# Performance work log

Measured on AMD Instinct MI355X. Metric: run time of the kernel, lower is better.

The kernel has to match this reference:

```python
import jax, jax.numpy as jnp
import numpy as np

B, S, H, D = 8, 1024, 16, 64
W = H * D  # hidden width = 1024


def setup_inputs() -> dict:
    key = jax.random.key(0)
    ks = jax.random.split(key, 5)
    std = 0.02
    return {
        "from_tensor": jax.random.normal(ks[0], (B, S, W), dtype=jnp.float32),
        "to_tensor": jax.random.normal(ks[1], (B, S, W), dtype=jnp.float32),
        "Wq": jax.random.normal(ks[2], (W, W), dtype=jnp.float32) * std,
        "bq": jnp.zeros((W,), dtype=jnp.float32),
        "Wk": jax.random.normal(ks[3], (W, W), dtype=jnp.float32) * std,
        "bk": jnp.zeros((W,), dtype=jnp.float32),
        "Wv": jax.random.normal(ks[4], (W, W), dtype=jnp.float32) * std,
        "bv": jnp.zeros((W,), dtype=jnp.float32),
    }


def reference(from_tensor, to_tensor, Wq, bq, Wk, bk, Wv, bv):
    # Q/K/V projections (no activations: query_act=key_act=value_act=None)
    q = from_tensor @ Wq + bq  # [B, S, W]
    k = to_tensor @ Wk + bk
    v = to_tensor @ Wv + bv
    # split heads -> [B, H, S, D]
    q = q.reshape(B, S, H, D).transpose(0, 2, 1, 3)
    k = k.reshape(B, S, H, D).transpose(0, 2, 1, 3)
    v = v.reshape(B, S, H, D).transpose(0, 2, 1, 3)
    scale = 1.0 / np.sqrt(float(D))
    scores = jnp.einsum("bhqd,bhkd->bhqk", q, k) * scale  # [B, H, S, S]
    # attention_mask=None, dropout_prob=0.0 -> no mask, no dropout
    probs = jax.nn.softmax(scores, axis=-1)
    ctx = jnp.einsum("bhqk,bhkd->bhqd", probs, v)  # [B, H, S, D]
    # merge heads -> [B, S, H*D] (do_return_2d_tensor=False)
    return ctx.transpose(0, 2, 1, 3).reshape(B, S, H * D)
```

## Files before the change

kernel.cpp:

```cpp
#include <hip/hip_runtime.h>
#include <hip/hip_bf16.h>
#include <math.h>


#define B_ 8
#define S_ 1024
#define H_ 16
#define D_ 64
#define W_ 1024

typedef __bf16 bf16x8 __attribute__((ext_vector_type(8)));
typedef float f32x4 __attribute__((ext_vector_type(4)));
typedef unsigned short ushort_t;

#define MFMA16(a, b, c) __builtin_amdgcn_mfma_f32_16x16x32_bf16((a), (b), (c), 0, 0, 0)

__device__ inline ushort_t f2bf(float f) {
    unsigned int u = __float_as_uint(f);
    u += 0x7fff + ((u >> 16) & 1);
    return (ushort_t)(u >> 16);
}

__device__ inline unsigned f2bf_rhu_u(float f) {
    return (__float_as_uint(f) + 0x8000u) >> 16;
}

__device__ inline void async16(const void* g, void* l) {
    __builtin_amdgcn_global_load_lds((const __attribute__((address_space(1))) void*)g,
                                     (__attribute__((address_space(3))) void*)l, 16, 0, 0);
}

__global__ __launch_bounds__(256) void prep(const float* __restrict__ from,
                                            const float* __restrict__ to_,
                                            const float* __restrict__ Wq,
                                            const float* __restrict__ Wk,
                                            const float* __restrict__ Wv,
                                            ushort_t* __restrict__ fromB,
                                            ushort_t* __restrict__ toB,
                                            ushort_t* __restrict__ Wt, int n4) {
    int z = blockIdx.y;
    int t = threadIdx.x;
    if (z < 2) {
        int i = blockIdx.x * 256 + t;
        if (i >= n4) return;
        const float* src = z ? to_ : from;
        ushort_t* dst = z ? toB : fromB;
        float4 v = ((const float4*)src)[i];
        ushort4 o;
        o.x = f2bf(v.x); o.y = f2bf(v.y); o.z = f2bf(v.z); o.w = f2bf(v.w);
        ((ushort4*)dst)[i] = o;
        return;
    }
    int bx = blockIdx.x;
    if (bx >= 3072) return;
    __shared__ float tile[32][33];
    int zz = bx >> 10;
    int tl = bx & 1023;
    int bxx = tl & 31, byy = tl >> 5;
    const float* src = (zz == 0) ? Wq : (zz == 1 ? Wk : Wv);
    ushort_t* dst = Wt + (size_t)zz * W_ * W_;
    int tx = t & 31, ty = t >> 5;
    int x = bxx * 32 + tx;
#pragma unroll
    for (int jj = 0; jj < 4; jj++) {
        int y = byy * 32 + ty + jj * 8;
        tile[ty + jj * 8][tx] = src[(size_t)y * W_ + x];
    }
    __syncthreads();
    int x2 = byy * 32 + tx;
#pragma unroll
    for (int jj = 0; jj < 4; jj++) {
        int y2 = bxx * 32 + ty + jj * 8;
        dst[(size_t)y2 * W_ + x2] = f2bf(tile[tx][ty + jj * 8]);
    }
}

__global__ __launch_bounds__(256) void qkv_gemm(const ushort_t* __restrict__ fromB,
                                                const ushort_t* __restrict__ toB,
                                                const ushort_t* __restrict__ Wt,
                                                const float* __restrict__ bq,
                                                const float* __restrict__ bk,
                                                const float* __restrict__ bv,
                                                ushort_t* __restrict__ Qd,
                                                ushort_t* __restrict__ Kd,
                                                ushort_t* __restrict__ Vt) {
    __shared__ __attribute__((aligned(16))) ushort_t As[128 * 32];
    __shared__ __attribute__((aligned(16))) ushort_t Bs[128 * 32];
    int z = blockIdx.y;
    const ushort_t* A = (z == 0) ? fromB : toB;
    const ushort_t* Bt = Wt + (size_t)z * (W_ * W_);
    const float* bias = (z == 0) ? bq : (z == 1 ? bk : bv);
    ushort_t* dst = (z == 0) ? Qd : (z == 1 ? Kd : Vt);

    int bx = blockIdx.x;
    int j64 = bx >> 3;
    int mTile = ((bx & 7) << 3) | (j64 >> 3);
    int nTile = j64 & 7;
    int mBase = mTile * 128, nBase = nTile * 128;

    int t = threadIdx.x;
    int lane = t & 63, w = t >> 6;
    int wm = w >> 1, wn = w & 1;
    int ln = lane & 15, qd = lane >> 4;
    int wb = t & ~63;

    f32x4 zero = {0.f, 0.f, 0.f, 0.f};
    f32x4 acc[4][4];
#pragma unroll
    for (int i = 0; i < 4; i++)
#pragma unroll
        for (int j = 0; j < 4; j++) acc[i][j] = zero;

    for (int kt = 0; kt < 32; ++kt) {
        int k0 = kt * 32;
#pragma unroll
        for (int c = 0; c < 2; ++c) {
            int idx16 = c * 256 + t;
            int row = idx16 >> 2, seg = idx16 & 3;
            async16(A + (size_t)(mBase + row) * W_ + k0 + seg * 8, As + (size_t)(c * 256 + wb) * 8);
            async16(Bt + (size_t)(nBase + row) * W_ + k0 + seg * 8, Bs + (size_t)(c * 256 + wb) * 8);
        }
        __syncthreads();
        bf16x8 af[4], bfr[4];
#pragma unroll
        for (int i = 0; i < 4; i++) af[i] = *(const bf16x8*)(As + (wm * 64 + i * 16 + ln) * 32 + qd * 8);
#pragma unroll
        for (int j = 0; j < 4; j++) bfr[j] = *(const bf16x8*)(Bs + (wn * 64 + j * 16 + ln) * 32 + qd * 8);
#pragma unroll
        for (int i = 0; i < 4; i++)
#pragma unroll
            for (int j = 0; j < 4; j++) acc[i][j] = MFMA16(af[i], bfr[j], acc[i][j]);
        __syncthreads();
    }

#pragma unroll
    for (int j = 0; j < 4; j++) {
        int n = nBase + wn * 64 + j * 16 + ln;
        float bb = bias[n];
        int h = n >> 6, d = n & 63;
#pragma unroll
        for (int i = 0; i < 4; i++) {
            int mrow = mBase + wm * 64 + i * 16 + qd * 4;
#pragma unroll
            for (int r = 0; r < 4; r++) {
                int m = mrow + r;
                int b = m >> 10, s = m & 1023;
                float v = acc[i][j][r] + bb;
                if (z == 0) v *= 0.18033688011111773f;
                size_t idx;
                if (z < 2) idx = ((size_t)(b * H_ + h) * S_ + s) * D_ + d;
                else {
                    int sp = (s & ~63) | (s & 0x23) | ((s & 0x0C) << 1) | ((s & 0x10) >> 2);
                    idx = ((size_t)(b * H_ + h) * D_ + d) * S_ + sp;
                }
                dst[idx] = f2bf(v);
            }
        }
    }
}

__global__ __launch_bounds__(256, 4) void attn(const ushort_t* __restrict__ Qd,
                                               const ushort_t* __restrict__ Kd,
                                               const ushort_t* __restrict__ Vt,
                                               float* __restrict__ out) {
    __shared__ __attribute__((aligned(16))) ushort_t Ks[2][4096];
    __shared__ __attribute__((aligned(16))) ushort_t Vs[2][4096];

    int L = blockIdx.x;
    int bh = ((L & 7) << 4) | ((L >> 3) & 15);
    int qx = L >> 7;
    int t = threadIdx.x, w = t >> 6, lane = t & 63;
    int ln = lane & 15, qd = lane >> 4;
    int qbase = qx * 128 + w * 32;
    const ushort_t* Qb = Qd + (size_t)bh * S_ * D_;
    const ushort_t* Kb = Kd + (size_t)bh * S_ * D_;
    const ushort_t* Vb = Vt + (size_t)bh * D_ * S_;

    bf16x8 qf[2][2];
#pragma unroll
    for (int i = 0; i < 2; i++) {
        const ushort_t* qp = Qb + (size_t)(qbase + i * 16 + ln) * D_ + qd * 8;
        qf[i][0] = *(const bf16x8*)qp;
        qf[i][1] = *(const bf16x8*)(qp + 32);
    }

    int l8 = lane >> 3, s8 = lane & 7;
    int stgOff = (s8 ^ l8) << 3;
    const ushort_t* kg = Kb + (size_t)(w * 16 + l8) * D_ + stgOff;
    const ushort_t* vg = Vb + (size_t)(w * 16 + l8) * S_ + stgOff;
    int kOff = ln * 64 + ((qd ^ (ln & 7)) << 3);

    float rs[2] = {0.f, 0.f};
    f32x4 zero = {0.f, 0.f, 0.f, 0.f};
    f32x4 accO[2][4];
#pragma unroll
    for (int i = 0; i < 2; i++)
#pragma unroll
        for (int jd = 0; jd < 4; jd++) accO[i][jd] = zero;

    async16(kg, &Ks[0][w * 1024]);
    async16(kg + 8 * D_, &Ks[0][w * 1024 + 512]);
    async16(vg, &Vs[0][w * 1024]);
    async16(vg + 8 * S_, &Vs[0][w * 1024 + 512]);

    for (int c = 0; c < 16; ++c) {
        int buf = c & 1;
        __builtin_amdgcn_s_waitcnt(0x0F70);
        __syncthreads();
        if (c + 1 < 16) {
            int kc = (c + 1) * 64;
            async16(kg + (size_t)kc * D_, &Ks[buf ^ 1][w * 1024]);
            async16(kg + (size_t)kc * D_ + 8 * D_, &Ks[buf ^ 1][w * 1024 + 512]);
            async16(vg + kc, &Vs[buf ^ 1][w * 1024]);
            async16(vg + kc + 8 * S_, &Vs[buf ^ 1][w * 1024 + 512]);
        }

        f32x4 sc[2][4];
#pragma unroll
        for (int i = 0; i < 2; i++)
#pragma unroll
            for (int j = 0; j < 4; j++) sc[i][j] = zero;
        __builtin_amdgcn_s_setprio(1);
#pragma unroll
        for (int j = 0; j < 4; j++) {
            bf16x8 k0 = *(const bf16x8*)&Ks[buf][j * 1024 + kOff];
            bf16x8 k1 = *(const bf16x8*)&Ks[buf][(j * 1024 + kOff) ^ 32];
#pragma unroll
            for (int i = 0; i < 2; i++) {
                sc[i][j] = MFMA16(k0, qf[i][0], sc[i][j]);
                sc[i][j] = MFMA16(k1, qf[i][1], sc[i][j]);
            }
        }
        __builtin_amdgcn_s_setprio(0);

        bf16x8 pfrag[2][2];
#pragma unroll
        for (int i = 0; i < 2; i++)
#pragma unroll
            for (int m = 0; m < 2; m++) {
                union { unsigned u[4]; bf16x8 v; } pk;
#pragma unroll
                for (int jh = 0; jh < 2; jh++) {
                    float p0 = exp2f(sc[i][2 * m + jh][0]);
                    float p1 = exp2f(sc[i][2 * m + jh][1]);
                    float p2 = exp2f(sc[i][2 * m + jh][2]);
                    float p3 = exp2f(sc[i][2 * m + jh][3]);
                    rs[i] += (p0 + p1) + (p2 + p3);
                    pk.u[jh * 2]     = f2bf_rhu_u(p0) | (f2bf_rhu_u(p1) << 16);
                    pk.u[jh * 2 + 1] = f2bf_rhu_u(p2) | (f2bf_rhu_u(p3) << 16);
                }
                pfrag[i][m] = pk.v;
            }

        __builtin_amdgcn_s_setprio(1);
#pragma unroll
        for (int dt = 0; dt < 4; dt++)
#pragma unroll
            for (int m = 0; m < 2; m++) {
                bf16x8 vf = *(const bf16x8*)&Vs[buf][(dt * 16 + ln) * 64 +
                                                    ((((m << 2) + qd) ^ (ln & 7)) << 3)];
                accO[0][dt] = MFMA16(vf, pfrag[0][m], accO[0][dt]);
                accO[1][dt] = MFMA16(vf, pfrag[1][m], accO[1][dt]);
            }
        __builtin_amdgcn_s_setprio(0);
    }

    float inv[2];
#pragma unroll
    for (int i = 0; i < 2; i++) {
        float s = rs[i];
        s += __shfl_xor(s, 16);
        s += __shfl_xor(s, 32);
        inv[i] = 1.f / s;
    }
    int b = bh >> 4, h = bh & 15;
#pragma unroll
    for (int i = 0; i < 2; i++) {
        int q = qbase + i * 16 + ln;
        float* op = out + ((size_t)(b * S_ + q) * H_ + h) * D_ + qd * 4;
#pragma unroll
        for (int dt = 0; dt < 4; dt++) {
            float4 o4;
            o4.x = accO[i][dt][0] * inv[i];
            o4.y = accO[i][dt][1] * inv[i];
            o4.z = accO[i][dt][2] * inv[i];
            o4.w = accO[i][dt][3] * inv[i];
            *(float4*)(op + dt * 16) = o4;
        }
    }
}

extern "C" void kernel_launch(void* const* d_in, const int* in_sizes, int n_in,
                              void* d_out, int out_size, void* d_ws, size_t ws_size,
                              hipStream_t stream) {
    const float* from = (const float*)d_in[0];
    const float* to_  = (const float*)d_in[1];
    const float* Wq = (const float*)d_in[2];
    const float* bq = (const float*)d_in[3];
    const float* Wk = (const float*)d_in[4];
    const float* bk = (const float*)d_in[5];
    const float* Wv = (const float*)d_in[6];
    const float* bv = (const float*)d_in[7];
    float* out = (float*)d_out;

    const size_t NTOK = (size_t)B_ * S_ * W_;
    ushort_t* ws = (ushort_t*)d_ws;
    ushort_t* fromB = ws;
    ushort_t* toB = fromB + NTOK;
    ushort_t* Wt = toB + NTOK;
    ushort_t* Qd = Wt + (size_t)3 * W_ * W_;
    ushort_t* Kd = Qd + NTOK;
    ushort_t* Vt = Kd + NTOK;

    int n4 = (int)(NTOK / 4);
    prep<<<dim3(n4 / 256, 3), dim3(256), 0, stream>>>(from, to_, Wq, Wk, Wv, fromB, toB, Wt, n4);
    qkv_gemm<<<dim3(512, 3), dim3(256), 0, stream>>>(fromB, toB, Wt, bq, bk, bv, Qd, Kd, Vt);
    attn<<<dim3(1024), dim3(256), 0, stream>>>(Qd, Kd, Vt, out);
}
```

Before: 262.0 us.

## Read K/V fragments directly from global memory and vectorize projection stores

The attention kernel drops its double-buffered LDS staging of K and V, along with the async copies and per-chunk barriers, and loads the MFMA fragments straight from global memory (relying on L2/L1 reuse across the four waves). The projection kernel swaps MFMA operand order for Q/K so that each lane holds four consecutive head-dim values. This lets Q/K/V outputs be written as 8-byte ushort4 stores with a vectorized bias load. The trade-off is that every wave now issues redundant global loads and may stall on memory latency that was previously hidden by prefetching.

```diff
diff --git a/kernel.cpp b/kernel.cpp
--- a/kernel.cpp
+++ b/kernel.cpp
@@ -126,34 +126,56 @@
         for (int i = 0; i < 4; i++) af[i] = *(const bf16x8*)(As + (wm * 64 + i * 16 + ln) * 32 + qd * 8);
 #pragma unroll
         for (int j = 0; j < 4; j++) bfr[j] = *(const bf16x8*)(Bs + (wn * 64 + j * 16 + ln) * 32 + qd * 8);
-#pragma unroll
-        for (int i = 0; i < 4; i++)
-#pragma unroll
-            for (int j = 0; j < 4; j++) acc[i][j] = MFMA16(af[i], bfr[j], acc[i][j]);
+        if (z < 2) {
+#pragma unroll
+            for (int i = 0; i < 4; i++)
+#pragma unroll
+                for (int j = 0; j < 4; j++) acc[i][j] = MFMA16(bfr[j], af[i], acc[i][j]);
+        } else {
+#pragma unroll
+            for (int i = 0; i < 4; i++)
+#pragma unroll
+                for (int j = 0; j < 4; j++) acc[i][j] = MFMA16(af[i], bfr[j], acc[i][j]);
+        }
         __syncthreads();
     }
 
-#pragma unroll
-    for (int j = 0; j < 4; j++) {
-        int n = nBase + wn * 64 + j * 16 + ln;
-        float bb = bias[n];
-        int h = n >> 6, d = n & 63;
-#pragma unroll
-        for (int i = 0; i < 4; i++) {
-            int mrow = mBase + wm * 64 + i * 16 + qd * 4;
-#pragma unroll
-            for (int r = 0; r < 4; r++) {
-                int m = mrow + r;
+    if (z < 2) {
+        float qs = (z == 0) ? 0.18033688011111773f : 1.0f;
+#pragma unroll
+        for (int j = 0; j < 4; j++) {
+            int n0 = nBase + wn * 64 + j * 16 + qd * 4;
+            float4 b4 = *(const float4*)&bias[n0];
+            int h = n0 >> 6, d0 = n0 & 63;
+#pragma unroll
+            for (int i = 0; i < 4; i++) {
+                int m = mBase + wm * 64 + i * 16 + ln;
                 int b = m >> 10, s = m & 1023;
-                float v = acc[i][j][r] + bb;
-                if (z == 0) v *= 0.18033688011111773f;
-                size_t idx;
-                if (z < 2) idx = ((size_t)(b * H_ + h) * S_ + s) * D_ + d;
-                else {
-                    int sp = (s & ~63) | (s & 0x23) | ((s & 0x0C) << 1) | ((s & 0x10) >> 2);
-                    idx = ((size_t)(b * H_ + h) * D_ + d) * S_ + sp;
-                }
-                dst[idx] = f2bf(v);
+                ushort4 o;
+                o.x = f2bf((acc[i][j][0] + b4.x) * qs);
+                o.y = f2bf((acc[i][j][1] + b4.y) * qs);
+                o.z = f2bf((acc[i][j][2] + b4.z) * qs);
+                o.w = f2bf((acc[i][j][3] + b4.w) * qs);
+                *(ushort4*)&dst[((size_t)(b * H_ + h) * S_ + s) * D_ + d0] = o;
+            }
+        }
+    } else {
+#pragma unroll
+        for (int j = 0; j < 4; j++) {
+            int n = nBase + wn * 64 + j * 16 + ln;
+            float bb = bias[n];
+            int h = n >> 6, d = n & 63;
+#pragma unroll
+            for (int i = 0; i < 4; i++) {
+                int s0 = mBase + wm * 64 + i * 16 + qd * 4;
+                int b = s0 >> 10, s = s0 & 1023;
+                int sp0 = (s & ~63) | (s & 0x23) | ((s & 0x0C) << 1) | ((s & 0x10) >> 2);
+                ushort4 o;
+                o.x = f2bf(acc[i][j][0] + bb);
+                o.y = f2bf(acc[i][j][1] + bb);
+                o.z = f2bf(acc[i][j][2] + bb);
+                o.w = f2bf(acc[i][j][3] + bb);
+                *(ushort4*)&dst[((size_t)(b * H_ + h) * D_ + d) * S_ + sp0] = o;
             }
         }
     }
@@ -163,9 +185,6 @@
                                                const ushort_t* __restrict__ Kd,
                                                const ushort_t* __restrict__ Vt,
                                                float* __restrict__ out) {
-    __shared__ __attribute__((aligned(16))) ushort_t Ks[2][4096];
-    __shared__ __attribute__((aligned(16))) ushort_t Vs[2][4096];
-
     int L = blockIdx.x;
     int bh = ((L & 7) << 4) | ((L >> 3) & 15);
     int qx = L >> 7;
@@ -184,11 +203,8 @@
         qf[i][1] = *(const bf16x8*)(qp + 32);
     }
 
-    int l8 = lane >> 3, s8 = lane & 7;
-    int stgOff = (s8 ^ l8) << 3;
-    const ushort_t* kg = Kb + (size_t)(w * 16 + l8) * D_ + stgOff;
-    const ushort_t* vg = Vb + (size_t)(w * 16 + l8) * S_ + stgOff;
-    int kOff = ln * 64 + ((qd ^ (ln & 7)) << 3);
+    const ushort_t* kp = Kb + (size_t)ln * D_ + qd * 8;
+    const ushort_t* vp0 = Vb + (size_t)ln * S_ + qd * 8;
 
     float rs[2] = {0.f, 0.f};
     f32x4 zero = {0.f, 0.f, 0.f, 0.f};
@@ -198,23 +214,7 @@
 #pragma unroll
         for (int jd = 0; jd < 4; jd++) accO[i][jd] = zero;
 
-    async16(kg, &Ks[0][w * 1024]);
-    async16(kg + 8 * D_, &Ks[0][w * 1024 + 512]);
-    async16(vg, &Vs[0][w * 1024]);
-    async16(vg + 8 * S_, &Vs[0][w * 1024 + 512]);
-
     for (int c = 0; c < 16; ++c) {
-        int buf = c & 1;
-        __builtin_amdgcn_s_waitcnt(0x0F70);
-        __syncthreads();
-        if (c + 1 < 16) {
-            int kc = (c + 1) * 64;
-            async16(kg + (size_t)kc * D_, &Ks[buf ^ 1][w * 1024]);
-            async16(kg + (size_t)kc * D_ + 8 * D_, &Ks[buf ^ 1][w * 1024 + 512]);
-            async16(vg + kc, &Vs[buf ^ 1][w * 1024]);
-            async16(vg + kc + 8 * S_, &Vs[buf ^ 1][w * 1024 + 512]);
-        }
-
         f32x4 sc[2][4];
 #pragma unroll
         for (int i = 0; i < 2; i++)
@@ -223,8 +223,9 @@
         __builtin_amdgcn_s_setprio(1);
 #pragma unroll
         for (int j = 0; j < 4; j++) {
-            bf16x8 k0 = *(const bf16x8*)&Ks[buf][j * 1024 + kOff];
-            bf16x8 k1 = *(const bf16x8*)&Ks[buf][(j * 1024 + kOff) ^ 32];
+            const ushort_t* kr = kp + (size_t)(c * 64 + j * 16) * D_;
+            bf16x8 k0 = *(const bf16x8*)kr;
+            bf16x8 k1 = *(const bf16x8*)(kr + 32);
 #pragma unroll
             for (int i = 0; i < 2; i++) {
                 sc[i][j] = MFMA16(k0, qf[i][0], sc[i][j]);
@@ -257,8 +258,7 @@
         for (int dt = 0; dt < 4; dt++)
 #pragma unroll
             for (int m = 0; m < 2; m++) {
-                bf16x8 vf = *(const bf16x8*)&Vs[buf][(dt * 16 + ln) * 64 +
-                                                    ((((m << 2) + qd) ^ (ln & 7)) << 3)];
+                bf16x8 vf = *(const bf16x8*)(vp0 + (size_t)dt * 16 * S_ + c * 64 + m * 32);
                 accO[0][dt] = MFMA16(vf, pfrag[0][m], accO[0][dt]);
                 accO[1][dt] = MFMA16(vf, pfrag[1][m], accO[1][dt]);
             }
```

Result: slower. 339.1 us (+29.4%).
